# Performance work log

Hardware: AMD Instinct MI355X
Metric: run time of the kernel (lower is better)

Reference implementation:

```python
import jax, jax.numpy as jnp
import numpy as np

D_IN, D_OUT, RANK, N = 4096, 4096, 16, 8192


def _quantize_weight(w, bits):
    # round-to-nearest fake quantization, stored back as floats (as in the torch code)
    absmax = jnp.abs(w).max()
    scale = (2 ** (bits - 1) - 1) / absmax
    q = jnp.clip(jnp.round(w * scale), -2 ** (bits - 1), 2 ** (bits - 1) - 1)
    return q / scale


def _double_quantization(w, bits):
    absmax = jnp.abs(w).max()
    c1 = (2 ** (bits - 1) - 1) / absmax          # scalar fp32 scale
    q = jnp.clip(jnp.round(w * c1), -2 ** (bits - 1), 2 ** (bits - 1) - 1)
    return c1, q / c1                             # c_kbit_2 has same shape as w


def setup_inputs() -> dict:
    key = jax.random.key(0)
    kX, kW, kL1, kL2 = jax.random.split(key, 4)
    X = jax.random.normal(kX, (N, D_IN), dtype=jnp.float32)
    W0 = jax.random.normal(kW, (D_IN, D_OUT), dtype=jnp.float32)
    W_nf4 = _quantize_weight(W0, bits=4)
    c_fp32_1, c_kbit_2 = _double_quantization(W_nf4, bits=8)
    L1 = jax.random.normal(kL1, (D_IN, RANK), dtype=jnp.float32)
    L2 = jax.random.normal(kL2, (RANK, D_OUT), dtype=jnp.float32)
    return {"X": X, "W_nf4": W_nf4, "c_fp32_1": c_fp32_1,
            "c_kbit_2": c_kbit_2, "L1": L1, "L2": L2}


def reference(X, W_nf4, c_fp32_1, c_kbit_2, L1, L2):
    # dequantize: elementwise scalar * elementwise-tensor scaling of stored weight
    W = W_nf4 * c_fp32_1 * c_kbit_2               # [D_IN, D_OUT]
    # main GEMM + low-rank LoRA path, added in the epilogue
    Y = X @ W + (X @ L1) @ L2                     # [N, D_OUT]
    return Y
```

## Files before the change

### kernel.cpp

```cpp
#include <hip/hip_runtime.h>


#define M_ROWS 8192
#define K_DIM  4096
#define N_OUT  4096
#define CVT_BLOCKS 16384
#define WP_BLOCKS  4096
#define XL1_BLOCKS 512
#define PREP_BLOCKS (CVT_BLOCKS + WP_BLOCKS + XL1_BLOCKS)

typedef float  f32x16 __attribute__((ext_vector_type(16)));
typedef float  f32x4  __attribute__((ext_vector_type(4)));
typedef __bf16 bf16x8 __attribute__((ext_vector_type(8)));
typedef unsigned short ushort8v __attribute__((ext_vector_type(8)));

__device__ float          Tg[(size_t)M_ROWS * 16];
__device__ unsigned short L1t[16 * K_DIM];
__device__ unsigned short L2t[N_OUT * 16];

__device__ __forceinline__ unsigned short f2bf(float f) {
    __bf16 h = (__bf16)f;
    union { __bf16 h; unsigned short u; } v; v.h = h;
    return v.u;
}

__global__ __launch_bounds__(256) void lorap_kernel(
        const float* __restrict__ L1, const float* __restrict__ L2) {
    const int idx = blockIdx.x * 256 + threadIdx.x;
    if (idx < K_DIM) {
        const float4* lp = (const float4*)&L1[(size_t)idx * 16];
        float4 r0 = lp[0], r1 = lp[1], r2 = lp[2], r3 = lp[3];
        float v[16] = {r0.x, r0.y, r0.z, r0.w, r1.x, r1.y, r1.z, r1.w,
                       r2.x, r2.y, r2.z, r2.w, r3.x, r3.y, r3.z, r3.w};
        #pragma unroll
        for (int r = 0; r < 16; ++r)
            L1t[(size_t)r * K_DIM + idx] = f2bf(v[r]);
    } else {
        const int n = idx - K_DIM;
        ushort8v a, b;
        #pragma unroll
        for (int r = 0; r < 8; ++r) a[r] = f2bf(L2[(size_t)r * N_OUT + n]);
        #pragma unroll
        for (int r = 0; r < 8; ++r) b[r] = f2bf(L2[(size_t)(r + 8) * N_OUT + n]);
        *(ushort8v*)&L2t[(size_t)n * 16]     = a;
        *(ushort8v*)&L2t[(size_t)n * 16 + 8] = b;
    }
}

__global__ __launch_bounds__(256) void prep_all_kernel(
        const float* __restrict__ X,    ushort8v* __restrict__ Xh,
        const float* __restrict__ Wnf4, const float* __restrict__ c1p,
        const float* __restrict__ c2,   unsigned short* __restrict__ Wt) {
    const int t = threadIdx.x;

    if (blockIdx.x < CVT_BLOCKS) {
        size_t tid = (size_t)blockIdx.x * 256 + t;
        const float4* xp = (const float4*)X;
        float4 a = xp[tid * 2];
        float4 b = xp[tid * 2 + 1];
        ushort8v o;
        o[0] = f2bf(a.x); o[1] = f2bf(a.y); o[2] = f2bf(a.z); o[3] = f2bf(a.w);
        o[4] = f2bf(b.x); o[5] = f2bf(b.y); o[6] = f2bf(b.z); o[7] = f2bf(b.w);
        Xh[tid] = o;
        return;
    }

    if (blockIdx.x < CVT_BLOCKS + WP_BLOCKS) {
        __shared__ unsigned short tile[64][72];
        const int wb = blockIdx.x - CVT_BLOCKS;
        const int n0 = (wb & 63) * 64;
        const int k0 = (wb >> 6) * 64;
        const float c1 = *c1p;

        #pragma unroll
        for (int i = 0; i < 4; ++i) {
            int idx = i * 1024 + t * 4;
            int k = idx >> 6, n4 = idx & 63;
            size_t g = (size_t)(k0 + k) * N_OUT + n0 + n4;
            float4 w = *(const float4*)&Wnf4[g];
            float4 s = *(const float4*)&c2[g];
            tile[n4    ][k] = f2bf(w.x * c1 * s.x);
            tile[n4 + 1][k] = f2bf(w.y * c1 * s.y);
            tile[n4 + 2][k] = f2bf(w.z * c1 * s.z);
            tile[n4 + 3][k] = f2bf(w.w * c1 * s.w);
        }
        __syncthreads();

        #pragma unroll
        for (int i = 0; i < 2; ++i) {
            int task = i * 256 + t;
            int n = task >> 3, k8 = (task & 7) * 8;
            ushort8v o = *(const ushort8v*)&tile[n][k8];
            *(ushort8v*)&Wt[(size_t)(n0 + n) * K_DIM + k0 + k8] = o;
        }
        return;
    }

    {
        __shared__ float red[4][256];
        const int m0 = (blockIdx.x - CVT_BLOCKS - WP_BLOCKS) * 16;
        const int wv = t >> 6, lane = t & 63;
        const int l15 = lane & 15, l4 = lane >> 4;
        const float* ap = X + (size_t)(m0 + l15) * K_DIM + wv * 1024 + l4 * 8;
        const __bf16* bp = (const __bf16*)L1t + (size_t)l15 * K_DIM + wv * 1024 + l4 * 8;
        f32x4 acc = {};
        #pragma unroll 8
        for (int k = 0; k < 1024; k += 32) {
            float4 p0 = *(const float4*)(ap + k);
            float4 p1 = *(const float4*)(ap + k + 4);
            bf16x8 a;
            a[0] = (__bf16)p0.x; a[1] = (__bf16)p0.y;
            a[2] = (__bf16)p0.z; a[3] = (__bf16)p0.w;
            a[4] = (__bf16)p1.x; a[5] = (__bf16)p1.y;
            a[6] = (__bf16)p1.z; a[7] = (__bf16)p1.w;
            bf16x8 b = *(const bf16x8*)(bp + k);
            acc = __builtin_amdgcn_mfma_f32_16x16x32_bf16(a, b, acc, 0, 0, 0);
        }
        #pragma unroll
        for (int r = 0; r < 4; ++r) red[wv][(l4 * 4 + r) * 16 + l15] = acc[r];
        __syncthreads();
        if (wv == 0) {
            #pragma unroll
            for (int r = 0; r < 4; ++r) {
                int e = (l4 * 4 + r) * 16 + l15;
                Tg[(size_t)(m0 + l4 * 4 + r) * 16 + l15] =
                    red[0][e] + red[1][e] + red[2][e] + red[3][e];
            }
        }
    }
}

#define COMPUTE(B) do { \
    bf16x8 af[2][2], bfr[2][2]; \
    _Pragma("unroll") for (int mt = 0; mt < 2; ++mt) \
      _Pragma("unroll") for (int ks = 0; ks < 2; ++ks) { \
        int row = wm + mt * 32 + l32; \
        int slot = (2 * ks + half) ^ rsw; \
        af[mt][ks] = *(const bf16x8*)(&As[B][0] + row * 32 + slot * 8); \
      } \
    _Pragma("unroll") for (int nt = 0; nt < 2; ++nt) \
      _Pragma("unroll") for (int ks = 0; ks < 2; ++ks) { \
        int row = wn + nt * 32 + l32; \
        int slot = (2 * ks + half) ^ rsw; \
        bfr[nt][ks] = *(const bf16x8*)(&Bs[B][0] + row * 32 + slot * 8); \
      } \
    _Pragma("unroll") for (int ks = 0; ks < 2; ++ks) \
      _Pragma("unroll") for (int mt = 0; mt < 2; ++mt) \
        _Pragma("unroll") for (int nt = 0; nt < 2; ++nt) \
          acc[mt][nt] = __builtin_amdgcn_mfma_f32_32x32x16_bf16( \
              af[mt][ks], bfr[nt][ks], acc[mt][nt], 0, 0, 0); \
} while (0)

__global__ __launch_bounds__(256) void gemm_bt_kernel(
        const __bf16* __restrict__ A, const __bf16* __restrict__ Bt,
        float* __restrict__ C, int m_base) {
    __shared__ __bf16 As[2][128 * 32];
    __shared__ __bf16 Bs[2][128 * 32];

    const int t    = threadIdx.x;
    const int w    = t >> 6;
    const int lane = t & 63;
    const int half = lane >> 5;
    const int l32  = lane & 31;

    const int m0   = m_base + blockIdx.y * 128;
    const int n0   = blockIdx.x * 128;

    const int wm   = (w >> 1) * 64;
    const int wn   = (w & 1) * 64;

    const int srow = lane >> 2;
    const int scol = ((lane & 3) ^ ((lane >> 3) & 3)) * 8;
    const int rsw = (l32 >> 1) & 3;

    f32x16 acc[2][2] = {};

    for (int kb = 0; kb < K_DIM; kb += 64) {
        __syncthreads();
        #pragma unroll
        for (int b = 0; b < 2; ++b) {
            #pragma unroll
            for (int j = 0; j < 2; ++j) {
                int row = w * 32 + j * 16 + srow;
                const __bf16* gp = A + (size_t)(m0 + row) * K_DIM + kb + b * 32 + scol;
                __builtin_amdgcn_global_load_lds(
                    (const __attribute__((address_space(1))) unsigned int*)gp,
                    (__attribute__((address_space(3))) unsigned int*)
                        (&As[b][0] + (w * 32 + j * 16) * 32),
                    16, 0, 0);
            }
            #pragma unroll
            for (int j = 0; j < 2; ++j) {
                int row = w * 32 + j * 16 + srow;
                const __bf16* gp = Bt + (size_t)(n0 + row) * K_DIM + kb + b * 32 + scol;
                __builtin_amdgcn_global_load_lds(
                    (const __attribute__((address_space(1))) unsigned int*)gp,
                    (__attribute__((address_space(3))) unsigned int*)
                        (&Bs[b][0] + (w * 32 + j * 16) * 32),
                    16, 0, 0);
            }
        }
        __syncthreads();

        COMPUTE(0);
        COMPUTE(1);
    }

    {
        bf16x8 afl[2], bfl[2];
        #pragma unroll
        for (int mt = 0; mt < 2; ++mt) {
            const float* tp = Tg + (size_t)(m0 + wm + mt * 32 + l32) * 16 + half * 8;
            float4 p0 = *(const float4*)tp;
            float4 p1 = *(const float4*)(tp + 4);
            afl[mt][0] = (__bf16)p0.x; afl[mt][1] = (__bf16)p0.y;
            afl[mt][2] = (__bf16)p0.z; afl[mt][3] = (__bf16)p0.w;
            afl[mt][4] = (__bf16)p1.x; afl[mt][5] = (__bf16)p1.y;
            afl[mt][6] = (__bf16)p1.z; afl[mt][7] = (__bf16)p1.w;
        }
        #pragma unroll
        for (int nt = 0; nt < 2; ++nt)
            bfl[nt] = *(const bf16x8*)((const __bf16*)L2t +
                        (size_t)(n0 + wn + nt * 32 + l32) * 16 + half * 8);
        #pragma unroll
        for (int mt = 0; mt < 2; ++mt)
            #pragma unroll
            for (int nt = 0; nt < 2; ++nt)
                acc[mt][nt] = __builtin_amdgcn_mfma_f32_32x32x16_bf16(
                    afl[mt], bfl[nt], acc[mt][nt], 0, 0, 0);
    }

    #pragma unroll
    for (int mt = 0; mt < 2; ++mt)
        #pragma unroll
        for (int nt = 0; nt < 2; ++nt) {
            int col = n0 + wn + nt * 32 + l32;
            #pragma unroll
            for (int reg = 0; reg < 16; ++reg) {
                int row = m0 + wm + mt * 32 + (reg & 3) + 8 * (reg >> 2) + 4 * half;
                C[(size_t)row * N_OUT + col] = acc[mt][nt][reg];
            }
        }
}

extern "C" void kernel_launch(void* const* d_in, const int* in_sizes, int n_in,
                              void* d_out, int out_size, void* d_ws, size_t ws_size,
                              hipStream_t stream) {
    const float* X    = (const float*)d_in[0];
    const float* Wnf4 = (const float*)d_in[1];
    const float* c1   = (const float*)d_in[2];
    const float* c2   = (const float*)d_in[3];
    const float* L1   = (const float*)d_in[4];
    const float* L2   = (const float*)d_in[5];
    float* Y = (float*)d_out;

    unsigned short* Xh = (unsigned short*)d_ws;
    unsigned short* Wt = (unsigned short*)((char*)d_ws + (size_t)M_ROWS * K_DIM * 2);

    lorap_kernel<<<32, 256, 0, stream>>>(L1, L2);
    prep_all_kernel<<<PREP_BLOCKS, 256, 0, stream>>>(
        X, (ushort8v*)Xh, Wnf4, c1, c2, Wt);

    for (int q = 0; q < 4; ++q)
        gemm_bt_kernel<<<dim3(N_OUT / 128, 16), 256, 0, stream>>>(
            (const __bf16*)Xh, (const __bf16*)Wt, Y, q * 2048);
}
```

Baseline: 720.5 us.

## Use persistent grid-stride prep blocks, split-K atomics for X·L1, fewer GEMM launches

The prep kernel now launches a fixed grid of persistent blocks that grid-stride over the X conversion, weight dequant-transpose and X·L1 work units, replacing one block per unit. The X·L1 low-rank product is split four ways along K and accumulated into Tg with atomicAdd, and Tg is zeroed in the LoRA prep kernel. The main GEMM is launched twice with 32 row-blocks each instead of four times with 16, cutting launch overhead and tail effects. The risks are atomic contention, nondeterministic summation order, and the zeroing of Tg depending on kernel ordering.

```diff
diff --git a/kernel.cpp b/kernel.cpp
--- a/kernel.cpp
+++ b/kernel.cpp
@@ -4,10 +4,14 @@
 #define M_ROWS 8192
 #define K_DIM  4096
 #define N_OUT  4096
-#define CVT_BLOCKS 16384
-#define WP_BLOCKS  4096
-#define XL1_BLOCKS 512
-#define PREP_BLOCKS (CVT_BLOCKS + WP_BLOCKS + XL1_BLOCKS)
+
+#define CVT_UNITS 16384
+#define WP_UNITS  4096
+#define XL1_UNITS 2048
+#define NCVT 1280
+#define NWP  512
+#define NXL  256
+#define PREP_GRID (NCVT + NWP + NXL)
 
 typedef float  f32x16 __attribute__((ext_vector_type(16)));
 typedef float  f32x4  __attribute__((ext_vector_type(4)));
@@ -27,6 +31,10 @@
 __global__ __launch_bounds__(256) void lorap_kernel(
         const float* __restrict__ L1, const float* __restrict__ L2) {
     const int idx = blockIdx.x * 256 + threadIdx.x;
+
+    #pragma unroll
+    for (int i = 0; i < 16; ++i) Tg[(size_t)idx * 16 + i] = 0.f;
+
     if (idx < K_DIM) {
         const float4* lp = (const float4*)&L1[(size_t)idx * 16];
         float4 r0 = lp[0], r1 = lp[1], r2 = lp[2], r3 = lp[3];
@@ -51,81 +59,88 @@
         const float* __restrict__ X,    ushort8v* __restrict__ Xh,
         const float* __restrict__ Wnf4, const float* __restrict__ c1p,
         const float* __restrict__ c2,   unsigned short* __restrict__ Wt) {
-    const int t = threadIdx.x;
-
-    if (blockIdx.x < CVT_BLOCKS) {
-        size_t tid = (size_t)blockIdx.x * 256 + t;
-        const float4* xp = (const float4*)X;
-        float4 a = xp[tid * 2];
-        float4 b = xp[tid * 2 + 1];
-        ushort8v o;
-        o[0] = f2bf(a.x); o[1] = f2bf(a.y); o[2] = f2bf(a.z); o[3] = f2bf(a.w);
-        o[4] = f2bf(b.x); o[5] = f2bf(b.y); o[6] = f2bf(b.z); o[7] = f2bf(b.w);
-        Xh[tid] = o;
+    const int t   = threadIdx.x;
+    const int bid = blockIdx.x;
+
+    if (bid < NCVT) {
+        for (int u = bid; u < CVT_UNITS; u += NCVT) {
+            size_t tid = (size_t)u * 256 + t;
+            const float4* xp = (const float4*)X;
+            float4 a = xp[tid * 2];
+            float4 b = xp[tid * 2 + 1];
+            ushort8v o;
+            o[0] = f2bf(a.x); o[1] = f2bf(a.y); o[2] = f2bf(a.z); o[3] = f2bf(a.w);
+            o[4] = f2bf(b.x); o[5] = f2bf(b.y); o[6] = f2bf(b.z); o[7] = f2bf(b.w);
+            Xh[tid] = o;
+        }
         return;
     }
 
-    if (blockIdx.x < CVT_BLOCKS + WP_BLOCKS) {
+    if (bid < NCVT + NWP) {
         __shared__ unsigned short tile[64][72];
-        const int wb = blockIdx.x - CVT_BLOCKS;
-        const int n0 = (wb & 63) * 64;
-        const int k0 = (wb >> 6) * 64;
         const float c1 = *c1p;
-
-        #pragma unroll
-        for (int i = 0; i < 4; ++i) {
-            int idx = i * 1024 + t * 4;
-            int k = idx >> 6, n4 = idx & 63;
-            size_t g = (size_t)(k0 + k) * N_OUT + n0 + n4;
-            float4 w = *(const float4*)&Wnf4[g];
-            float4 s = *(const float4*)&c2[g];
-            tile[n4    ][k] = f2bf(w.x * c1 * s.x);
-            tile[n4 + 1][k] = f2bf(w.y * c1 * s.y);
-            tile[n4 + 2][k] = f2bf(w.z * c1 * s.z);
-            tile[n4 + 3][k] = f2bf(w.w * c1 * s.w);
-        }
-        __syncthreads();
-
-        #pragma unroll
-        for (int i = 0; i < 2; ++i) {
-            int task = i * 256 + t;
-            int n = task >> 3, k8 = (task & 7) * 8;
-            ushort8v o = *(const ushort8v*)&tile[n][k8];
-            *(ushort8v*)&Wt[(size_t)(n0 + n) * K_DIM + k0 + k8] = o;
+        for (int wb = bid - NCVT; wb < WP_UNITS; wb += NWP) {
+            const int n0 = (wb & 63) * 64;
+            const int k0 = (wb >> 6) * 64;
+            #pragma unroll
+            for (int i = 0; i < 4; ++i) {
+                int idx = i * 1024 + t * 4;
+                int k = idx >> 6, n4 = idx & 63;
+                size_t g = (size_t)(k0 + k) * N_OUT + n0 + n4;
+                float4 w = *(const float4*)&Wnf4[g];
+                float4 s = *(const float4*)&c2[g];
+                tile[n4    ][k] = f2bf(w.x * c1 * s.x);
+                tile[n4 + 1][k] = f2bf(w.y * c1 * s.y);
+                tile[n4 + 2][k] = f2bf(w.z * c1 * s.z);
+                tile[n4 + 3][k] = f2bf(w.w * c1 * s.w);
+            }
+            __syncthreads();
+            #pragma unroll
+            for (int i = 0; i < 2; ++i) {
+                int task = i * 256 + t;
+                int n = task >> 3, k8 = (task & 7) * 8;
+                ushort8v o = *(const ushort8v*)&tile[n][k8];
+                *(ushort8v*)&Wt[(size_t)(n0 + n) * K_DIM + k0 + k8] = o;
+            }
+            __syncthreads();
         }
         return;
     }
 
     {
         __shared__ float red[4][256];
-        const int m0 = (blockIdx.x - CVT_BLOCKS - WP_BLOCKS) * 16;
         const int wv = t >> 6, lane = t & 63;
         const int l15 = lane & 15, l4 = lane >> 4;
-        const float* ap = X + (size_t)(m0 + l15) * K_DIM + wv * 1024 + l4 * 8;
-        const __bf16* bp = (const __bf16*)L1t + (size_t)l15 * K_DIM + wv * 1024 + l4 * 8;
-        f32x4 acc = {};
-        #pragma unroll 8
-        for (int k = 0; k < 1024; k += 32) {
-            float4 p0 = *(const float4*)(ap + k);
-            float4 p1 = *(const float4*)(ap + k + 4);
-            bf16x8 a;
-            a[0] = (__bf16)p0.x; a[1] = (__bf16)p0.y;
-            a[2] = (__bf16)p0.z; a[3] = (__bf16)p0.w;
-            a[4] = (__bf16)p1.x; a[5] = (__bf16)p1.y;
-            a[6] = (__bf16)p1.z; a[7] = (__bf16)p1.w;
-            bf16x8 b = *(const bf16x8*)(bp + k);
-            acc = __builtin_amdgcn_mfma_f32_16x16x32_bf16(a, b, acc, 0, 0, 0);
-        }
-        #pragma unroll
-        for (int r = 0; r < 4; ++r) red[wv][(l4 * 4 + r) * 16 + l15] = acc[r];
-        __syncthreads();
-        if (wv == 0) {
-            #pragma unroll
-            for (int r = 0; r < 4; ++r) {
-                int e = (l4 * 4 + r) * 16 + l15;
-                Tg[(size_t)(m0 + l4 * 4 + r) * 16 + l15] =
-                    red[0][e] + red[1][e] + red[2][e] + red[3][e];
-            }
+        for (int u = bid - NCVT - NWP; u < XL1_UNITS; u += NXL) {
+            const int m0 = (u >> 2) * 16;
+            const int kb = (u & 3) * 1024 + wv * 256;
+            const float* ap = X + (size_t)(m0 + l15) * K_DIM + kb + l4 * 8;
+            const __bf16* bp = (const __bf16*)L1t + (size_t)l15 * K_DIM + kb + l4 * 8;
+            f32x4 acc = {};
+            #pragma unroll
+            for (int k = 0; k < 256; k += 32) {
+                float4 p0 = *(const float4*)(ap + k);
+                float4 p1 = *(const float4*)(ap + k + 4);
+                bf16x8 a;
+                a[0] = (__bf16)p0.x; a[1] = (__bf16)p0.y;
+                a[2] = (__bf16)p0.z; a[3] = (__bf16)p0.w;
+                a[4] = (__bf16)p1.x; a[5] = (__bf16)p1.y;
+                a[6] = (__bf16)p1.z; a[7] = (__bf16)p1.w;
+                bf16x8 b = *(const bf16x8*)(bp + k);
+                acc = __builtin_amdgcn_mfma_f32_16x16x32_bf16(a, b, acc, 0, 0, 0);
+            }
+            #pragma unroll
+            for (int r = 0; r < 4; ++r) red[wv][(l4 * 4 + r) * 16 + l15] = acc[r];
+            __syncthreads();
+            if (wv == 0) {
+                #pragma unroll
+                for (int r = 0; r < 4; ++r) {
+                    int e = (l4 * 4 + r) * 16 + l15;
+                    atomicAdd(&Tg[(size_t)(m0 + l4 * 4 + r) * 16 + l15],
+                              red[0][e] + red[1][e] + red[2][e] + red[3][e]);
+                }
+            }
+            __syncthreads();
         }
     }
 }
@@ -258,10 +273,11 @@
     unsigned short* Wt = (unsigned short*)((char*)d_ws + (size_t)M_ROWS * K_DIM * 2);
 
     lorap_kernel<<<32, 256, 0, stream>>>(L1, L2);
-    prep_all_kernel<<<PREP_BLOCKS, 256, 0, stream>>>(
+    prep_all_kernel<<<PREP_GRID, 256, 0, stream>>>(
         X, (ushort8v*)Xh, Wnf4, c1, c2, Wt);
 
-    for (int q = 0; q < 4; ++q)
-        gemm_bt_kernel<<<dim3(N_OUT / 128, 16), 256, 0, stream>>>(
-            (const __bf16*)Xh, (const __bf16*)Wt, Y, q * 2048);
-}
+    gemm_bt_kernel<<<dim3(N_OUT / 128, 32), 256, 0, stream>>>(
+        (const __bf16*)Xh, (const __bf16*)Wt, Y, 0);
+    gemm_bt_kernel<<<dim3(N_OUT / 128, 32), 256, 0, stream>>>(
+        (const __bf16*)Xh, (const __bf16*)Wt, Y, 4096);
+}
```

Result: no change. 713.9 us (-0.9%).

## Fuse X bf16 conversion into X@L1 pass and merge GEMM launches

Applied to the files above, without the earlier changes.

The separate X-to-bf16 conversion blocks are removed. The X@L1 low-rank blocks already read fp32 X and convert it, so they now also write the bf16 copy. This drops one full read of X (128MB of fp32). The main GEMM also goes from four launches of 16 row-blocks to two launches of 32, which cuts launch overhead and tail effects. The risk is that the 512 XL1 blocks become the serial bottleneck, with few blocks each doing large per-thread strided stores.

```diff
diff --git a/kernel.cpp b/kernel.cpp
--- a/kernel.cpp
+++ b/kernel.cpp
@@ -4,10 +4,8 @@
 #define M_ROWS 8192
 #define K_DIM  4096
 #define N_OUT  4096
-#define CVT_BLOCKS 16384
+#define XL1_BLOCKS 512
 #define WP_BLOCKS  4096
-#define XL1_BLOCKS 512
-#define PREP_BLOCKS (CVT_BLOCKS + WP_BLOCKS + XL1_BLOCKS)
 
 typedef float  f32x16 __attribute__((ext_vector_type(16)));
 typedef float  f32x4  __attribute__((ext_vector_type(4)));
@@ -48,60 +46,19 @@
 }
 
 __global__ __launch_bounds__(256) void prep_all_kernel(
-        const float* __restrict__ X,    ushort8v* __restrict__ Xh,
+        const float* __restrict__ X,    unsigned short* __restrict__ Xh,
         const float* __restrict__ Wnf4, const float* __restrict__ c1p,
         const float* __restrict__ c2,   unsigned short* __restrict__ Wt) {
     const int t = threadIdx.x;
 
-    if (blockIdx.x < CVT_BLOCKS) {
-        size_t tid = (size_t)blockIdx.x * 256 + t;
-        const float4* xp = (const float4*)X;
-        float4 a = xp[tid * 2];
-        float4 b = xp[tid * 2 + 1];
-        ushort8v o;
-        o[0] = f2bf(a.x); o[1] = f2bf(a.y); o[2] = f2bf(a.z); o[3] = f2bf(a.w);
-        o[4] = f2bf(b.x); o[5] = f2bf(b.y); o[6] = f2bf(b.z); o[7] = f2bf(b.w);
-        Xh[tid] = o;
-        return;
-    }
-
-    if (blockIdx.x < CVT_BLOCKS + WP_BLOCKS) {
-        __shared__ unsigned short tile[64][72];
-        const int wb = blockIdx.x - CVT_BLOCKS;
-        const int n0 = (wb & 63) * 64;
-        const int k0 = (wb >> 6) * 64;
-        const float c1 = *c1p;
-
-        #pragma unroll
-        for (int i = 0; i < 4; ++i) {
-            int idx = i * 1024 + t * 4;
-            int k = idx >> 6, n4 = idx & 63;
-            size_t g = (size_t)(k0 + k) * N_OUT + n0 + n4;
-            float4 w = *(const float4*)&Wnf4[g];
-            float4 s = *(const float4*)&c2[g];
-            tile[n4    ][k] = f2bf(w.x * c1 * s.x);
-            tile[n4 + 1][k] = f2bf(w.y * c1 * s.y);
-            tile[n4 + 2][k] = f2bf(w.z * c1 * s.z);
-            tile[n4 + 3][k] = f2bf(w.w * c1 * s.w);
-        }
-        __syncthreads();
-
-        #pragma unroll
-        for (int i = 0; i < 2; ++i) {
-            int task = i * 256 + t;
-            int n = task >> 3, k8 = (task & 7) * 8;
-            ushort8v o = *(const ushort8v*)&tile[n][k8];
-            *(ushort8v*)&Wt[(size_t)(n0 + n) * K_DIM + k0 + k8] = o;
-        }
-        return;
-    }
-
-    {
+    if (blockIdx.x < XL1_BLOCKS) {
         __shared__ float red[4][256];
-        const int m0 = (blockIdx.x - CVT_BLOCKS - WP_BLOCKS) * 16;
+        const int m0 = blockIdx.x * 16;
         const int wv = t >> 6, lane = t & 63;
         const int l15 = lane & 15, l4 = lane >> 4;
-        const float* ap = X + (size_t)(m0 + l15) * K_DIM + wv * 1024 + l4 * 8;
+        const size_t rowoff = (size_t)(m0 + l15) * K_DIM + wv * 1024 + l4 * 8;
+        const float* ap = X + rowoff;
+        unsigned short* xp = Xh + rowoff;
         const __bf16* bp = (const __bf16*)L1t + (size_t)l15 * K_DIM + wv * 1024 + l4 * 8;
         f32x4 acc = {};
         #pragma unroll 8
@@ -113,6 +70,7 @@
             a[2] = (__bf16)p0.z; a[3] = (__bf16)p0.w;
             a[4] = (__bf16)p1.x; a[5] = (__bf16)p1.y;
             a[6] = (__bf16)p1.z; a[7] = (__bf16)p1.w;
+            *(bf16x8*)(xp + k) = a;
             bf16x8 b = *(const bf16x8*)(bp + k);
             acc = __builtin_amdgcn_mfma_f32_16x16x32_bf16(a, b, acc, 0, 0, 0);
         }
@@ -126,6 +84,37 @@
                 Tg[(size_t)(m0 + l4 * 4 + r) * 16 + l15] =
                     red[0][e] + red[1][e] + red[2][e] + red[3][e];
             }
+        }
+        return;
+    }
+
+    {
+        __shared__ unsigned short tile[64][72];
+        const int wb = blockIdx.x - XL1_BLOCKS;
+        const int n0 = (wb & 63) * 64;
+        const int k0 = (wb >> 6) * 64;
+        const float c1 = *c1p;
+
+        #pragma unroll
+        for (int i = 0; i < 4; ++i) {
+            int idx = i * 1024 + t * 4;
+            int k = idx >> 6, n4 = idx & 63;
+            size_t g = (size_t)(k0 + k) * N_OUT + n0 + n4;
+            float4 w = *(const float4*)&Wnf4[g];
+            float4 s = *(const float4*)&c2[g];
+            tile[n4    ][k] = f2bf(w.x * c1 * s.x);
+            tile[n4 + 1][k] = f2bf(w.y * c1 * s.y);
+            tile[n4 + 2][k] = f2bf(w.z * c1 * s.z);
+            tile[n4 + 3][k] = f2bf(w.w * c1 * s.w);
+        }
+        __syncthreads();
+
+        #pragma unroll
+        for (int i = 0; i < 2; ++i) {
+            int task = i * 256 + t;
+            int n = task >> 3, k8 = (task & 7) * 8;
+            ushort8v o = *(const ushort8v*)&tile[n][k8];
+            *(ushort8v*)&Wt[(size_t)(n0 + n) * K_DIM + k0 + k8] = o;
         }
     }
 }
@@ -258,10 +247,11 @@
     unsigned short* Wt = (unsigned short*)((char*)d_ws + (size_t)M_ROWS * K_DIM * 2);
 
     lorap_kernel<<<32, 256, 0, stream>>>(L1, L2);
-    prep_all_kernel<<<PREP_BLOCKS, 256, 0, stream>>>(
-        X, (ushort8v*)Xh, Wnf4, c1, c2, Wt);
-
-    for (int q = 0; q < 4; ++q)
-        gemm_bt_kernel<<<dim3(N_OUT / 128, 16), 256, 0, stream>>>(
-            (const __bf16*)Xh, (const __bf16*)Wt, Y, q * 2048);
-}
+    prep_all_kernel<<<XL1_BLOCKS + WP_BLOCKS, 256, 0, stream>>>(
+        X, Xh, Wnf4, c1, c2, Wt);
+
+    gemm_bt_kernel<<<dim3(N_OUT / 128, 32), 256, 0, stream>>>(
+        (const __bf16*)Xh, (const __bf16*)Wt, Y, 0);
+    gemm_bt_kernel<<<dim3(N_OUT / 128, 32), 256, 0, stream>>>(
+        (const __bf16*)Xh, (const __bf16*)Wt, Y, 4096);
+}
```

New measurement: 636.3 us. -11.7%, faster.
